# Kernel optimization log

Measured on AMD Instinct MI355X. Metric: run time of the kernel, lower is better.

Reference implementation:

```python
import jax, jax.numpy as jnp
import numpy as np

TEMPERATURE = 8.0  # sqrt(head_dim=64)
NEG_INF = -1e9


def setup_inputs() -> dict:
    key = jax.random.key(0)
    k1, k2, k3, k4, k5 = jax.random.split(key, 5)
    B, H, S, D = 1, 8, 2048, 64
    q = jax.random.normal(k1, (B, H, S, D), dtype=jnp.float32)
    k = jax.random.normal(k2, (B, H, S, D), dtype=jnp.float32)
    v = jax.random.normal(k3, (B, H, S, D), dtype=jnp.float32)
    sph = jax.random.uniform(k4, (B, H, S, S), dtype=jnp.float32)
    mask = jax.random.randint(k5, (B, H, S, S), 0, 2, dtype=jnp.int32)
    return {"q": q, "k": k, "v": v, "sph": sph, "mask": mask}


def reference(q, k, v, sph, mask):
    # scores: [B,H,Sq,Sk]
    attn = jnp.einsum('bhqd,bhkd->bhqk', q / TEMPERATURE, k)
    attn = attn * sph                       # multiplicative bias
    attn = jnp.where(mask == 0, NEG_INF, attn)
    p_attn = jax.nn.softmax(attn, axis=-1)  # dropout p=0 -> identity
    out = jnp.einsum('bhqk,bhkd->bhqd', p_attn, v)
    return (out, p_attn)
```

## Files before the change

kernel.cpp:

```cpp
#include <hip/hip_runtime.h>

#define SLEN 2048
#define DIM  64
#define NH   8
#define TQ   16
#define NEG_INF -1e9f

typedef __attribute__((ext_vector_type(8))) short short8;
typedef __attribute__((ext_vector_type(4))) float f32x4;
typedef unsigned short ushort;

__device__ inline ushort f2bf(float x) {
    unsigned u = __float_as_uint(x);
    u += 0x7fffu + ((u >> 16) & 1u);
    return (ushort)(u >> 16);
}
__device__ inline float bf2f(ushort b) {
    return __uint_as_float(((unsigned)b) << 16);
}

__global__ __launch_bounds__(256)
void convk_kernel(const float* __restrict__ k,
                  ushort* __restrict__ khi, ushort* __restrict__ klo)
{
    int i4 = blockIdx.x * 256 + threadIdx.x;
    float4 x = ((const float4*)k)[i4];
    ushort h0 = f2bf(x.x), h1 = f2bf(x.y), h2 = f2bf(x.z), h3 = f2bf(x.w);
    ushort4 hi = {h0, h1, h2, h3};
    ushort4 lo = {f2bf(x.x - bf2f(h0)), f2bf(x.y - bf2f(h1)),
                  f2bf(x.z - bf2f(h2)), f2bf(x.w - bf2f(h3))};
    ((ushort4*)khi)[i4] = hi;
    ((ushort4*)klo)[i4] = lo;
}

__global__ __launch_bounds__(256)
void convv_kernel(const float* __restrict__ v, ushort* __restrict__ vt)
{
    __shared__ ushort sT[64][70];
    const int h  = blockIdx.x >> 5;
    const int st = blockIdx.x & 31;
    const int t  = threadIdx.x;
    {
        const int r0 = t >> 4;
        const int c  = (t & 15) * 4;
        #pragma unroll
        for (int rr = r0; rr < 64; rr += 16) {
            float4 x = *(const float4*)(v + ((size_t)(h * SLEN + st * 64 + rr)) * DIM + c);
            sT[c + 0][rr] = f2bf(x.x);
            sT[c + 1][rr] = f2bf(x.y);
            sT[c + 2][rr] = f2bf(x.z);
            sT[c + 3][rr] = f2bf(x.w);
        }
    }
    __syncthreads();
    {
        const int d  = t >> 2;
        const int s0 = (t & 3) * 16;
        short8 a = *(const short8*)(&sT[d][s0]);
        short8 b = *(const short8*)(&sT[d][s0 + 8]);
        ushort* dst = vt + ((size_t)(h * DIM + d)) * SLEN + st * 64 + s0;
        *(short8*)(dst)     = a;
        *(short8*)(dst + 8) = b;
    }
}

__global__ __launch_bounds__(512, 2)
void attn_mfma_kernel(const float* __restrict__ q,
                      const ushort* __restrict__ khi,
                      const ushort* __restrict__ klo,
                      const ushort* __restrict__ vt,
                      const float* __restrict__ sph,
                      const int*   __restrict__ mask,
                      float* __restrict__ out,
                      float* __restrict__ p_out)
{
    __shared__ ushort sP[TQ][SLEN + 8];
    __shared__ ushort sQhi[TQ][72];
    __shared__ ushort sQlo[TQ][72];
    __shared__ float sMax[TQ][8];
    __shared__ float sSum[TQ][8];
    __shared__ float sC[4][TQ][16];

    const int tid  = threadIdx.x;
    const int wave = tid >> 6;
    const int lane = tid & 63;
    const int quad = lane >> 4;
    const int l16  = lane & 15;
    const int bx0  = blockIdx.x;
    const int bx   = ((bx0 & 7) << 7) | (bx0 >> 3);
    const int h    = bx >> 7;
    const int qr0  = (bx & 127) * TQ;

    {
        int e = tid * 2;
        int r = e >> 6, d = e & 63;
        float2 qv = *(const float2*)(q + ((size_t)(h * SLEN + qr0 + r)) * DIM + d);
        ushort h0 = f2bf(qv.x), h1 = f2bf(qv.y);
        sQhi[r][d]     = h0;
        sQhi[r][d + 1] = h1;
        sQlo[r][d]     = f2bf(qv.x - bf2f(h0));
        sQlo[r][d + 1] = f2bf(qv.y - bf2f(h1));
    }
    __syncthreads();

    short8 ah0 = *(const short8*)(&sQhi[l16][quad * 8]);
    short8 ah1 = *(const short8*)(&sQhi[l16][32 + quad * 8]);
    short8 al0 = *(const short8*)(&sQlo[l16][quad * 8]);
    short8 al1 = *(const short8*)(&sQlo[l16][32 + quad * 8]);

    const int n0 = wave * 256;

    unsigned ro[4];
    #pragma unroll
    for (int j = 0; j < 4; ++j)
        ro[j] = (unsigned)((h * SLEN + qr0 + quad * 4 + j) * SLEN + n0 + l16);

    float sv[8][4];
    int   mv[8][4];
    #pragma unroll
    for (int t = 0; t < 8; ++t) {
        #pragma unroll
        for (int j = 0; j < 4; ++j) {
            sv[t][j] = __builtin_nontemporal_load(sph  + ro[j] + t * 16);
            mv[t][j] = __builtin_nontemporal_load(mask + ro[j] + t * 16);
        }
    }

    f32x4 c[16];
    #pragma unroll
    for (int t = 0; t < 16; ++t) c[t] = (f32x4){0.f, 0.f, 0.f, 0.f};

    float rmax[4] = {-3.4e38f, -3.4e38f, -3.4e38f, -3.4e38f};

    #pragma unroll
    for (int t = 0; t < 16; ++t) {
        const size_t rowb = ((size_t)(h * SLEN + n0 + t * 16 + l16)) * DIM + quad * 8;
        short8 bh0 = *(const short8*)(khi + rowb);
        short8 bh1 = *(const short8*)(khi + rowb + 32);
        short8 bl0 = *(const short8*)(klo + rowb);
        short8 bl1 = *(const short8*)(klo + rowb + 32);
        c[t] = __builtin_amdgcn_mfma_f32_16x16x32_bf16(ah0, bh0, c[t], 0, 0, 0);
        c[t] = __builtin_amdgcn_mfma_f32_16x16x32_bf16(ah1, bh1, c[t], 0, 0, 0);
        c[t] = __builtin_amdgcn_mfma_f32_16x16x32_bf16(ah0, bl0, c[t], 0, 0, 0);
        c[t] = __builtin_amdgcn_mfma_f32_16x16x32_bf16(ah1, bl1, c[t], 0, 0, 0);
        c[t] = __builtin_amdgcn_mfma_f32_16x16x32_bf16(al0, bh0, c[t], 0, 0, 0);
        c[t] = __builtin_amdgcn_mfma_f32_16x16x32_bf16(al1, bh1, c[t], 0, 0, 0);

        const int slot = t & 7;
        #pragma unroll
        for (int j = 0; j < 4; ++j) {
            float s = c[t][j] * 0.125f * sv[slot][j];
            s = (mv[slot][j] == 0) ? NEG_INF : s;
            c[t][j] = s;
            rmax[j] = fmaxf(rmax[j], s);
        }
        if (t + 8 < 16) {
            #pragma unroll
            for (int j = 0; j < 4; ++j) {
                sv[slot][j] = __builtin_nontemporal_load(sph  + ro[j] + (t + 8) * 16);
                mv[slot][j] = __builtin_nontemporal_load(mask + ro[j] + (t + 8) * 16);
            }
        }
    }

    #pragma unroll
    for (int off = 1; off <= 8; off <<= 1) {
        #pragma unroll
        for (int j = 0; j < 4; ++j)
            rmax[j] = fmaxf(rmax[j], __shfl_xor(rmax[j], off));
    }
    if (l16 == 0) {
        #pragma unroll
        for (int j = 0; j < 4; ++j) sMax[quad * 4 + j][wave] = rmax[j];
    }
    __syncthreads();

    float M[4];
    #pragma unroll
    for (int j = 0; j < 4; ++j) {
        float m = sMax[quad * 4 + j][0];
        #pragma unroll
        for (int w = 1; w < 8; ++w) m = fmaxf(m, sMax[quad * 4 + j][w]);
        M[j] = m;
    }

    float rsum[4] = {0.f, 0.f, 0.f, 0.f};
    #pragma unroll
    for (int t = 0; t < 16; ++t) {
        #pragma unroll
        for (int j = 0; j < 4; ++j) {
            float e = __expf(c[t][j] - M[j]);
            c[t][j] = e;
            rsum[j] += e;
        }
    }
    #pragma unroll
    for (int off = 1; off <= 8; off <<= 1) {
        #pragma unroll
        for (int j = 0; j < 4; ++j)
            rsum[j] += __shfl_xor(rsum[j], off);
    }
    if (l16 == 0) {
        #pragma unroll
        for (int j = 0; j < 4; ++j) sSum[quad * 4 + j][wave] = rsum[j];
    }
    __syncthreads();

    float inv[4];
    #pragma unroll
    for (int j = 0; j < 4; ++j) {
        float s = 0.f;
        #pragma unroll
        for (int w = 0; w < 8; ++w) s += sSum[quad * 4 + j][w];
        inv[j] = 1.0f / s;
    }

    #pragma unroll
    for (int t = 0; t < 16; ++t) {
        #pragma unroll
        for (int j = 0; j < 4; ++j) {
            const int row = quad * 4 + j;
            const int col = n0 + t * 16 + l16;
            float p = c[t][j] * inv[j];
            p_out[ro[j] + t * 16] = p;
            sP[row][col] = f2bf(p);
        }
    }
    __syncthreads();

    const int ntile = wave & 3;
    const int khalf = wave >> 2;
    f32x4 o = (f32x4){0.f, 0.f, 0.f, 0.f};
    const ushort* vb = vt + ((size_t)(h * DIM + ntile * 16 + l16)) * SLEN
                          + khalf * 1024 + quad * 8;
    #pragma unroll 8
    for (int s = 0; s < 32; ++s) {
        short8 a = *(const short8*)(&sP[l16][khalf * 1024 + s * 32 + quad * 8]);
        short8 b = *(const short8*)(vb + s * 32);
        o = __builtin_amdgcn_mfma_f32_16x16x32_bf16(a, b, o, 0, 0, 0);
    }
    if (wave >= 4) {
        #pragma unroll
        for (int j = 0; j < 4; ++j) sC[ntile][quad * 4 + j][l16] = o[j];
    }
    __syncthreads();
    if (wave < 4) {
        #pragma unroll
        for (int j = 0; j < 4; ++j) {
            float r = o[j] + sC[ntile][quad * 4 + j][l16];
            out[((size_t)(h * SLEN) + qr0 + quad * 4 + j) * DIM + ntile * 16 + l16] = r;
        }
    }
}

extern "C" void kernel_launch(void* const* d_in, const int* in_sizes, int n_in,
                              void* d_out, int out_size, void* d_ws, size_t ws_size,
                              hipStream_t stream) {
    const float* q    = (const float*)d_in[0];
    const float* k    = (const float*)d_in[1];
    const float* v    = (const float*)d_in[2];
    const float* sph  = (const float*)d_in[3];
    const int*   mask = (const int*)d_in[4];
    float* out   = (float*)d_out;
    float* p_out = out + (size_t)NH * SLEN * DIM;

    const size_t nkv = (size_t)NH * SLEN * DIM;
    ushort* khi = (ushort*)d_ws;
    ushort* klo = khi + nkv;
    ushort* vt  = klo + nkv;

    hipLaunchKernelGGL(convk_kernel, dim3(nkv / 4 / 256), dim3(256), 0, stream,
                       k, khi, klo);
    hipLaunchKernelGGL(convv_kernel, dim3(NH * (SLEN / 64)), dim3(256), 0, stream,
                       v, vt);
    hipLaunchKernelGGL(attn_mfma_kernel, dim3(NH * (SLEN / TQ)), dim3(512), 0, stream,
                       q, khi, klo, vt, sph, mask, out, p_out);
}
```

Measured before the change: 397.5 us.

## Pack mask into bits in a prepass and stage sph through LDS with coalesced loads

A new prepass kernel reads the int32 mask and packs it into 16-bit bitmask words. The attention kernel then reads only the small bitmask instead of per-element int loads. The sph bias is now loaded as full-row coalesced float4 vectors, staged through a new shared-memory buffer in two halves, and read back per MFMA fragment. Column ownership is split into two 128-column strips per wave, and p_out stores are moved after the barrier. The trade-off is an extra full pass over the mask, a second kernel launch, and roughly 66 KB more LDS per block, which may lower occupancy.

```diff
diff --git a/kernel.cpp b/kernel.cpp
--- a/kernel.cpp
+++ b/kernel.cpp
@@ -64,17 +64,35 @@
     }
 }
 
+__global__ __launch_bounds__(256)
+void convm_kernel(const int* __restrict__ mask, ushort* __restrict__ mb)
+{
+    size_t i = (size_t)blockIdx.x * 256 + threadIdx.x;
+    const int4* p = (const int4*)(mask + i * 16);
+    unsigned m = 0;
+    #pragma unroll
+    for (int w = 0; w < 4; ++w) {
+        int4 a = p[w];
+        m |= (a.x != 0 ? 1u : 0u) << (w * 4 + 0);
+        m |= (a.y != 0 ? 1u : 0u) << (w * 4 + 1);
+        m |= (a.z != 0 ? 1u : 0u) << (w * 4 + 2);
+        m |= (a.w != 0 ? 1u : 0u) << (w * 4 + 3);
+    }
+    mb[i] = (ushort)m;
+}
+
 __global__ __launch_bounds__(512, 2)
 void attn_mfma_kernel(const float* __restrict__ q,
                       const ushort* __restrict__ khi,
                       const ushort* __restrict__ klo,
                       const ushort* __restrict__ vt,
                       const float* __restrict__ sph,
-                      const int*   __restrict__ mask,
+                      const unsigned* __restrict__ mbits,
                       float* __restrict__ out,
                       float* __restrict__ p_out)
 {
     __shared__ ushort sP[TQ][SLEN + 8];
+    __shared__ float  sS[TQ][1024 + 4];
     __shared__ ushort sQhi[TQ][72];
     __shared__ ushort sQlo[TQ][72];
     __shared__ float sMax[TQ][8];
@@ -108,33 +126,44 @@
     short8 al0 = *(const short8*)(&sQlo[l16][quad * 8]);
     short8 al1 = *(const short8*)(&sQlo[l16][32 + quad * 8]);
 
-    const int n0 = wave * 256;
-
-    unsigned ro[4];
-    #pragma unroll
-    for (int j = 0; j < 4; ++j)
-        ro[j] = (unsigned)((h * SLEN + qr0 + quad * 4 + j) * SLEN + n0 + l16);
-
-    float sv[8][4];
-    int   mv[8][4];
-    #pragma unroll
-    for (int t = 0; t < 8; ++t) {
-        #pragma unroll
-        for (int j = 0; j < 4; ++j) {
-            sv[t][j] = __builtin_nontemporal_load(sph  + ro[j] + t * 16);
-            mv[t][j] = __builtin_nontemporal_load(mask + ro[j] + t * 16);
-        }
-    }
+    const int cb0 = wave * 128;
+    const int cb1 = 1024 + wave * 128;
+
+    unsigned roA[4], roB[4];
+    #pragma unroll
+    for (int j = 0; j < 4; ++j) {
+        unsigned rb = (unsigned)((h * SLEN + qr0 + quad * 4 + j) * SLEN);
+        roA[j] = rb + cb0 + l16;
+        roB[j] = rb + cb1 + l16;
+    }
+
+    unsigned mwA[4][4], mwB[4][4];
+    #pragma unroll
+    for (int j = 0; j < 4; ++j) {
+        const unsigned* mr = mbits
+            + (size_t)(h * SLEN + qr0 + quad * 4 + j) * (SLEN / 32);
+        *(uint4*)mwA[j] = *(const uint4*)(mr + (cb0 >> 5));
+        *(uint4*)mwB[j] = *(const uint4*)(mr + (cb1 >> 5));
+    }
+
+    const int srow = wave * 2;
+    f32x4 g0[8];
+    #pragma unroll
+    for (int r = 0; r < 2; ++r)
+        #pragma unroll
+        for (int i = 0; i < 4; ++i)
+            g0[r * 4 + i] = __builtin_nontemporal_load(
+                (const f32x4*)(sph + (size_t)(h * SLEN + qr0 + srow + r) * SLEN
+                                   + i * 256 + lane * 4));
 
     f32x4 c[16];
     #pragma unroll
     for (int t = 0; t < 16; ++t) c[t] = (f32x4){0.f, 0.f, 0.f, 0.f};
 
-    float rmax[4] = {-3.4e38f, -3.4e38f, -3.4e38f, -3.4e38f};
-
     #pragma unroll
     for (int t = 0; t < 16; ++t) {
-        const size_t rowb = ((size_t)(h * SLEN + n0 + t * 16 + l16)) * DIM + quad * 8;
+        const int cb = (t < 8) ? (cb0 + t * 16) : (cb1 + (t - 8) * 16);
+        const size_t rowb = ((size_t)(h * SLEN + cb + l16)) * DIM + quad * 8;
         short8 bh0 = *(const short8*)(khi + rowb);
         short8 bh1 = *(const short8*)(khi + rowb + 32);
         short8 bl0 = *(const short8*)(klo + rowb);
@@ -145,21 +174,57 @@
         c[t] = __builtin_amdgcn_mfma_f32_16x16x32_bf16(ah1, bl1, c[t], 0, 0, 0);
         c[t] = __builtin_amdgcn_mfma_f32_16x16x32_bf16(al0, bh0, c[t], 0, 0, 0);
         c[t] = __builtin_amdgcn_mfma_f32_16x16x32_bf16(al1, bh1, c[t], 0, 0, 0);
-
-        const int slot = t & 7;
-        #pragma unroll
-        for (int j = 0; j < 4; ++j) {
-            float s = c[t][j] * 0.125f * sv[slot][j];
-            s = (mv[slot][j] == 0) ? NEG_INF : s;
+    }
+
+    #pragma unroll
+    for (int r = 0; r < 2; ++r)
+        #pragma unroll
+        for (int i = 0; i < 4; ++i)
+            *(f32x4*)&sS[srow + r][i * 256 + lane * 4] = g0[r * 4 + i];
+    __syncthreads();
+
+    f32x4 g1[8];
+    #pragma unroll
+    for (int r = 0; r < 2; ++r)
+        #pragma unroll
+        for (int i = 0; i < 4; ++i)
+            g1[r * 4 + i] = __builtin_nontemporal_load(
+                (const f32x4*)(sph + (size_t)(h * SLEN + qr0 + srow + r) * SLEN
+                                   + 1024 + i * 256 + lane * 4));
+
+    float rmax[4] = {-3.4e38f, -3.4e38f, -3.4e38f, -3.4e38f};
+    #pragma unroll
+    for (int t = 0; t < 8; ++t) {
+        #pragma unroll
+        for (int j = 0; j < 4; ++j) {
+            float sphv = sS[quad * 4 + j][cb0 + t * 16 + l16];
+            float s = c[t][j] * 0.125f * sphv;
+            const unsigned ok = (mwA[j][t >> 1] >> ((t & 1) * 16 + l16)) & 1u;
+            s = ok ? s : NEG_INF;
             c[t][j] = s;
             rmax[j] = fmaxf(rmax[j], s);
         }
-        if (t + 8 < 16) {
-            #pragma unroll
-            for (int j = 0; j < 4; ++j) {
-                sv[slot][j] = __builtin_nontemporal_load(sph  + ro[j] + (t + 8) * 16);
-                mv[slot][j] = __builtin_nontemporal_load(mask + ro[j] + (t + 8) * 16);
-            }
+    }
+    __syncthreads();
+
+    #pragma unroll
+    for (int r = 0; r < 2; ++r)
+        #pragma unroll
+        for (int i = 0; i < 4; ++i)
+            *(f32x4*)&sS[srow + r][i * 256 + lane * 4] = g1[r * 4 + i];
+    __syncthreads();
+
+    #pragma unroll
+    for (int t = 8; t < 16; ++t) {
+        #pragma unroll
+        for (int j = 0; j < 4; ++j) {
+            float sphv = sS[quad * 4 + j][cb0 + (t - 8) * 16 + l16];
+            float s = c[t][j] * 0.125f * sphv;
+            const unsigned ok =
+                (mwB[j][(t - 8) >> 1] >> (((t - 8) & 1) * 16 + l16)) & 1u;
+            s = ok ? s : NEG_INF;
+            c[t][j] = s;
+            rmax[j] = fmaxf(rmax[j], s);
         }
     }
 
@@ -219,14 +284,20 @@
     for (int t = 0; t < 16; ++t) {
         #pragma unroll
         for (int j = 0; j < 4; ++j) {
-            const int row = quad * 4 + j;
-            const int col = n0 + t * 16 + l16;
+            const int col = ((t < 8) ? (cb0 + t * 16) : (cb1 + (t - 8) * 16)) + l16;
             float p = c[t][j] * inv[j];
-            p_out[ro[j] + t * 16] = p;
-            sP[row][col] = f2bf(p);
-        }
-    }
-    __syncthreads();
+            c[t][j] = p;
+            sP[quad * 4 + j][col] = f2bf(p);
+        }
+    }
+    __syncthreads();
+
+    #pragma unroll
+    for (int t = 0; t < 16; ++t) {
+        #pragma unroll
+        for (int j = 0; j < 4; ++j)
+            p_out[(t < 8) ? (roA[j] + t * 16) : (roB[j] + (t - 8) * 16)] = c[t][j];
+    }
 
     const int ntile = wave & 3;
     const int khalf = wave >> 2;
@@ -268,11 +339,16 @@
     ushort* khi = (ushort*)d_ws;
     ushort* klo = khi + nkv;
     ushort* vt  = klo + nkv;
+    ushort* mbits = vt + nkv;
+
+    const size_t nmask = (size_t)NH * SLEN * SLEN;
 
     hipLaunchKernelGGL(convk_kernel, dim3(nkv / 4 / 256), dim3(256), 0, stream,
                        k, khi, klo);
     hipLaunchKernelGGL(convv_kernel, dim3(NH * (SLEN / 64)), dim3(256), 0, stream,
                        v, vt);
+    hipLaunchKernelGGL(convm_kernel, dim3(nmask / 16 / 256), dim3(256), 0, stream,
+                       mask, mbits);
     hipLaunchKernelGGL(attn_mfma_kernel, dim3(NH * (SLEN / TQ)), dim3(512), 0, stream,
-                       q, khi, klo, vt, sph, mask, out, p_out);
-}
+                       q, khi, klo, vt, sph, (const unsigned*)mbits, out, p_out);
+}
```

Result: slower. 415.5 us (+4.5%).
